# Optimization experiments

Hardware: AMD Instinct MI355X
Metric: run time of the kernel (lower is better)

Reference implementation:

```python
import jax, jax.numpy as jnp
import numpy as np

N_RAYS = 4096
WORLD_LEN = 160
K0_DIM = 12
WIDTH = 128
VIEWPE = 4
BG_LEN = 0.2
XYZ_MIN = -1.0 - BG_LEN
XYZ_MAX = 1.0 + BG_LEN
ALPHA_INIT = 1e-4
ACT_SHIFT = float(np.log(1.0 / (1.0 - ALPHA_INIT) - 1.0))  # density bias shift
BG = 1.0  # background color (render_kwargs['bg'])
DIM0 = 3 + 3 * VIEWPE * 2 + K0_DIM  # 39


def grid_interp(grid, pts):
    """Trilinear interpolation (align_corners=True). grid: [C,R,R,R], pts: [M,3] world coords -> [M,C]."""
    R = grid.shape[1]
    g = (pts - XYZ_MIN) / (XYZ_MAX - XYZ_MIN) * (R - 1)
    g = jnp.clip(g, 0.0, R - 1)
    g0 = jnp.clip(jnp.floor(g).astype(jnp.int32), 0, R - 2)
    f = g - g0
    x0, y0, z0 = g0[:, 0], g0[:, 1], g0[:, 2]
    fx, fy, fz = f[:, 0], f[:, 1], f[:, 2]

    def gat(i, j, k):
        return grid[:, i, j, k]  # [C, M]

    c00 = gat(x0, y0, z0) * (1 - fz) + gat(x0, y0, z0 + 1) * fz
    c01 = gat(x0, y0 + 1, z0) * (1 - fz) + gat(x0, y0 + 1, z0 + 1) * fz
    c10 = gat(x0 + 1, y0, z0) * (1 - fz) + gat(x0 + 1, y0, z0 + 1) * fz
    c11 = gat(x0 + 1, y0 + 1, z0) * (1 - fz) + gat(x0 + 1, y0 + 1, z0 + 1) * fz
    c0 = c00 * (1 - fy) + c01 * fy
    c1 = c10 * (1 - fy) + c11 * fy
    return (c0 * (1 - fx) + c1 * fx).T  # [M, C]


def setup_inputs() -> dict:
    key = jax.random.key(0)
    ks = jax.random.split(key, 11)
    return {
        "rays_o": jax.random.normal(ks[0], (N_RAYS, 3), jnp.float32) * 0.3,
        "rays_d": jax.random.normal(ks[1], (N_RAYS, 3), jnp.float32),
        "viewdirs": jax.random.normal(ks[2], (N_RAYS, 3), jnp.float32),
        "density_grid": jax.random.normal(ks[3], (1, WORLD_LEN, WORLD_LEN, WORLD_LEN), jnp.float32),
        "k0_grid": jax.random.normal(ks[4], (K0_DIM, WORLD_LEN, WORLD_LEN, WORLD_LEN), jnp.float32),
        "w0": jax.random.normal(ks[5], (DIM0, WIDTH), jnp.float32) * 0.05,
        "b0": jnp.zeros((WIDTH,), jnp.float32),
        "w1": jax.random.normal(ks[6], (WIDTH, WIDTH), jnp.float32) * 0.05,
        "b1": jnp.zeros((WIDTH,), jnp.float32),
        "w2": jax.random.normal(ks[7], (WIDTH, 3), jnp.float32) * 0.05,
        "b2": jnp.zeros((3,), jnp.float32),
        "stepsize": 1,
    }


def reference(rays_o, rays_d, viewdirs, density_grid, k0_grid, w0, b0, w1, b1, w2, b2, stepsize):
    sqrt3 = float(np.sqrt(3.0))
    # --- sample_ray: sample points along rays in the contracted domain ---
    N_inner = int(2.0 / (2.0 + 2.0 * BG_LEN) * sqrt3 * WORLD_LEN / stepsize) + 1
    N_outer = int(N_inner * max(0.01, BG_LEN / 2.0))
    b_inner = jnp.linspace(0.0, 2.0 * sqrt3, N_inner + 1)
    b_outer = 2.0 * sqrt3 / jnp.linspace(1.0, 0.001, N_outer + 1)
    t = jnp.concatenate([(b_inner[1:] + b_inner[:-1]) * 0.5,
                         (b_outer[1:] + b_outer[:-1]) * 0.5])  # [P]
    # scene_center = 0, scene_radius = 1 for xyz_min=-1, xyz_max=1
    rd = rays_d / jnp.linalg.norm(rays_d, axis=-1, keepdims=True)
    pts = rays_o[:, None, :] + rd[:, None, :] * t[None, :, None]  # [N,P,3]
    norm = jnp.max(jnp.abs(pts), axis=-1, keepdims=True)
    safe = jnp.maximum(norm, 1e-9)
    pts = jnp.where(norm <= 1.0, pts, pts / safe * (1.0 + BG_LEN - BG_LEN / safe))
    N, P = pts.shape[0], pts.shape[1]
    flat = pts.reshape(-1, 3)  # [M,3]

    # --- density -> alpha (Raw2Alpha); mask_cache is all-True, fast_color_thres=0 ---
    interval = float(stepsize) * 1.0  # voxel_size_ratio == 1
    dens = grid_interp(density_grid, flat)[:, 0].reshape(N, P)
    alpha = 1.0 - jnp.power(1.0 + jnp.exp(dens + ACT_SHIFT), -interval)

    # --- Alphas2Weights: per-ray alpha compositing ---
    T = jnp.cumprod(1.0 - alpha, axis=1)
    T_excl = jnp.concatenate([jnp.ones((N, 1), T.dtype), T[:, :-1]], axis=1)
    weights = alpha * T_excl  # [N,P]
    alphainv_last = T[:, -1]  # [N]

    # --- k0 features + view-dependent MLP ---
    k0 = grid_interp(k0_grid, flat).reshape(N, P, K0_DIM)
    vf = (2.0 ** jnp.arange(VIEWPE)).astype(rays_o.dtype)
    ve = (viewdirs[..., None] * vf).reshape(N, -1)
    vemb = jnp.concatenate([viewdirs, jnp.sin(ve), jnp.cos(ve)], axis=-1)  # [N, 3+24]
    feat = jnp.concatenate(
        [k0, jnp.broadcast_to(vemb[:, None, :], (N, P, vemb.shape[-1]))], axis=-1)  # [N,P,39]
    h = jax.nn.relu(feat @ w0 + b0)
    h = jax.nn.relu(h @ w1 + b1)
    rgb = jax.nn.sigmoid(h @ w2 + b2)  # [N,P,3]

    # --- volume rendering ---
    rgb_marched = jnp.sum(weights[..., None] * rgb, axis=1) + alphainv_last[:, None] * BG
    return rgb_marched  # [N,3]
```

## Files before the change

### kernel.cpp

```cpp
#include <hip/hip_runtime.h>

#define NRAYS 4096
#define PSAMP 254
#define NIN   231
#define GR    160
#define GR2   25600
#define GR3   4096000
#define SROW  136

typedef __attribute__((ext_vector_type(8))) short bf16x8;
typedef __attribute__((ext_vector_type(4))) float f32x4;

__device__ __forceinline__ unsigned short f2bf(float x) {
    union { float f; unsigned u; } v; v.f = x;
    return (unsigned short)((v.u + 0x7fffu + ((v.u >> 16) & 1u)) >> 16);
}
__device__ __forceinline__ float sigmoidf_(float x) { return 1.0f / (1.0f + __expf(-x)); }

__device__ __forceinline__ unsigned cvt_pk_bf16(float a, float b) {
    unsigned r;
    asm("v_cvt_pk_bf16_f32 %0, %1, %2" : "=v"(r) : "v"(a), "v"(b));
    return r;
}

__device__ __forceinline__ unsigned packh2(float a, float b) {
    union { _Float16 h; unsigned short u; } ua, ub;
    ua.h = (_Float16)a; ub.h = (_Float16)b;
    return (unsigned)ua.u | ((unsigned)ub.u << 16);
}
__device__ __forceinline__ float h2f(unsigned u16) {
    union { unsigned short u; _Float16 h; } v; v.u = (unsigned short)u16;
    return (float)v.h;
}
__device__ __forceinline__ float cget(const uint4& q, int c) {
    const unsigned w = ((const unsigned*)&q)[c >> 1];
    return h2f((c & 1) ? (w >> 16) : (w & 0xffffu));
}

__global__ void prepack(const float* __restrict__ w, unsigned short* __restrict__ out,
                        int K, int N, int ldw, int NT, int KS) {
    const int idx = blockIdx.x * 256 + threadIdx.x;
    if (idx >= NT * KS * 64) return;
    const int l  = idx & 63, f = idx >> 6;
    const int ks = f % KS,  nt = f / KS;
    const int n  = nt * 16 + (l & 15);
    const int k0 = ks * 32 + (l >> 4) * 8;
    unsigned p[4];
    #pragma unroll
    for (int q = 0; q < 4; q++) {
        const int ka = k0 + 2 * q, kb = ka + 1;
        const float va = (ka < K && n < N) ? w[ka * ldw + n] : 0.0f;
        const float vb = (kb < K && n < N) ? w[kb * ldw + n] : 0.0f;
        p[q] = (unsigned)f2bf(va) | ((unsigned)f2bf(vb) << 16);
    }
    uint4 v; v.x = p[0]; v.y = p[1]; v.z = p[2]; v.w = p[3];
    ((uint4*)out)[idx] = v;
}

__global__ __launch_bounds__(256) void repack_grid(
    const float* __restrict__ dg, const float* __restrict__ k0g,
    unsigned short* __restrict__ pg)
{
    const int i2 = blockIdx.x * 256 + threadIdx.x;
    if (i2 >= GR3 / 2) return;
    unsigned ow[16];
    #pragma unroll
    for (int c = 0; c < 12; c += 2) {
        const float2 va = ((const float2*)(k0g + (size_t)c       * GR3))[i2];
        const float2 vb = ((const float2*)(k0g + (size_t)(c + 1) * GR3))[i2];
        ow[(c >> 1)]     = packh2(va.x, vb.x);
        ow[8 + (c >> 1)] = packh2(va.y, vb.y);
    }
    const float2 dv = ((const float2*)dg)[i2];
    ow[6]  = packh2(dv.x, 0.0f);
    ow[14] = packh2(dv.y, 0.0f);
    ow[7] = 0u; ow[15] = 0u;
    uint4* dst = (uint4*)(pg + (size_t)i2 * 32);
    dst[0] = make_uint4(ow[0],  ow[1],  ow[2],  ow[3]);
    dst[1] = make_uint4(ow[4],  ow[5],  ow[6],  ow[7]);
    dst[2] = make_uint4(ow[8],  ow[9],  ow[10], ow[11]);
    dst[3] = make_uint4(ow[12], ow[13], ow[14], ow[15]);
}

__global__ __launch_bounds__(256, 2) void voxgo_mfma_pk(
    const float* __restrict__ rays_o, const float* __restrict__ rays_d,
    const float* __restrict__ viewdirs,
    const unsigned short* __restrict__ pg,
    const float* __restrict__ b0, const float* __restrict__ b1,
    const float* __restrict__ b2,
    const unsigned short* __restrict__ pw0, const unsigned short* __restrict__ pw1,
    const unsigned short* __restrict__ pw2,
    float* __restrict__ out)
{
    const int r    = blockIdx.x;
    const int tid  = threadIdx.x;
    const int wv   = tid >> 6, lane = tid & 63, quad = lane >> 4, l16 = lane & 15;

    __shared__ unsigned short hbuf[4][64 * SROW];
    __shared__ float wgt[256];
    __shared__ float redbuf[4 * 16 * 3];
    __shared__ float wtot[4];

    const float ox = rays_o[3*r+0], oy = rays_o[3*r+1], oz = rays_o[3*r+2];
    float dxv = rays_d[3*r+0], dyv = rays_d[3*r+1], dzv = rays_d[3*r+2];
    const float vdx = viewdirs[3*r+0], vdy = viewdirs[3*r+1], vdz = viewdirs[3*r+2];
    const float rinv = rsqrtf(dxv*dxv + dyv*dyv + dzv*dzv);
    dxv *= rinv; dyv *= rinv; dzv *= rinv;

    float t;
    if (tid < NIN) {
        t = ((float)tid + 0.5f) * (2.0f * 1.7320508075688772f / 231.0f);
    } else {
        const float lstep = 0.999f / 23.0f;
        const int j = tid - NIN;
        const float L0 = 1.0f - (float)j * lstep;
        const float L1 = 1.0f - (float)(j+1) * lstep;
        t = 1.7320508075688772f * (1.0f/L0 + 1.0f/L1);
    }

    float px = fmaf(dxv, t, ox), py = fmaf(dyv, t, oy), pz = fmaf(dzv, t, oz);
    const float nrm = fmaxf(fabsf(px), fmaxf(fabsf(py), fabsf(pz)));
    if (nrm > 1.0f) {
        const float s = (1.2f - 0.2f / nrm) / nrm;
        px *= s; py *= s; pz *= s;
    }

    const float gsc = 159.0f / 2.4f;
    const float gx = fminf(fmaxf((px + 1.2f) * gsc, 0.0f), 159.0f);
    const float gy = fminf(fmaxf((py + 1.2f) * gsc, 0.0f), 159.0f);
    const float gz = fminf(fmaxf((pz + 1.2f) * gsc, 0.0f), 159.0f);
    const int x0 = min((int)gx, GR-2), y0 = min((int)gy, GR-2), z0 = min((int)gz, GR-2);
    const float fx = gx - (float)x0, fy = gy - (float)y0, fz = gz - (float)z0;
    const int base = x0*GR2 + y0*GR + z0;

    const unsigned short* cp = pg + (size_t)base * 16;
    uint4 hi[8], lo[8];
    #pragma unroll
    for (int j = 0; j < 8; j++) {
        const int off = ((j >> 2) * GR2 + ((j >> 1) & 1) * GR + (j & 1)) * 16;
        hi[j] = *((const uint4*)(cp + off) + 1);
    }
    #pragma unroll
    for (int j = 0; j < 8; j++) {
        const int off = ((j >> 2) * GR2 + ((j >> 1) & 1) * GR + (j & 1)) * 16;
        lo[j] = *((const uint4*)(cp + off));
    }

    float fv[40];
    fv[12] = vdx; fv[13] = vdy; fv[14] = vdz;
    #pragma unroll
    for (int p = 0; p < 4; p++) {
        const float f = (float)(1 << p);
        fv[15+p] = __sinf(vdx*f);  fv[19+p] = __sinf(vdy*f);  fv[23+p] = __sinf(vdz*f);
        fv[27+p] = __cosf(vdx*f);  fv[31+p] = __cosf(vdy*f);  fv[35+p] = __cosf(vdz*f);
    }
    fv[39] = 0.0f;

    float dcr[8];
    #pragma unroll
    for (int j = 0; j < 8; j++) dcr[j] = h2f(hi[j].z & 0xffffu);
    const float c00 = dcr[0]*(1.0f-fz) + dcr[1]*fz;
    const float c01 = dcr[2]*(1.0f-fz) + dcr[3]*fz;
    const float c10 = dcr[4]*(1.0f-fz) + dcr[5]*fz;
    const float c11 = dcr[6]*(1.0f-fz) + dcr[7]*fz;
    const float dens = (c00*(1.0f-fy) + c01*fy)*(1.0f-fx) + (c10*(1.0f-fy) + c11*fy)*fx;

    const float ACT_SHIFT = -9.21024036697535f;
    const float alpha = (tid < PSAMP) ? sigmoidf_(dens + ACT_SHIFT) : 0.0f;

    float vscan = 1.0f - alpha;
    #pragma unroll
    for (int off = 1; off < 64; off <<= 1) {
        const float u = __shfl_up(vscan, off);
        if (lane >= off) vscan *= u;
    }
    if (lane == 63) wtot[wv] = vscan;
    __syncthreads();
    float pre = 1.0f;
    #pragma unroll
    for (int w = 0; w < 3; w++) if (w < wv) pre *= wtot[w];
    const float eprev = __shfl_up(vscan, 1);
    const float T_excl = (lane == 0) ? pre : pre * eprev;
    wgt[tid] = alpha * T_excl;

    const float wx0 = 1.0f-fx, wy0 = 1.0f-fy, wz0 = 1.0f-fz;
    const float w000 = wx0*wy0*wz0, w001 = wx0*wy0*fz, w010 = wx0*fy*wz0, w011 = wx0*fy*fz;
    const float w100 = fx*wy0*wz0,  w101 = fx*wy0*fz,  w110 = fx*fy*wz0,  w111 = fx*fy*fz;

    #pragma unroll
    for (int c = 0; c < 12; c++) {
        float s;
        if (c < 8) {
            s = w000*cget(lo[0],c) + w001*cget(lo[1],c)
              + w010*cget(lo[2],c) + w011*cget(lo[3],c)
              + w100*cget(lo[4],c) + w101*cget(lo[5],c)
              + w110*cget(lo[6],c) + w111*cget(lo[7],c);
        } else {
            s = w000*cget(hi[0],c-8) + w001*cget(hi[1],c-8)
              + w010*cget(hi[2],c-8) + w011*cget(hi[3],c-8)
              + w100*cget(hi[4],c-8) + w101*cget(hi[5],c-8)
              + w110*cget(hi[6],c-8) + w111*cget(hi[7],c-8);
        }
        fv[c] = s;
    }

    unsigned short* hb = &hbuf[wv][0];
    {
        const int row = tid & 63;
        uint4* dst = (uint4*)(hb + row * SROW);
        #pragma unroll
        for (int i = 0; i < 8; i++) {
            unsigned p[4];
            #pragma unroll
            for (int q = 0; q < 4; q++) {
                const int e0 = i*8 + 2*q, e1 = e0 + 1;
                const float a = (e0 < 39) ? fv[e0] : 0.0f;
                const float b = (e1 < 39) ? fv[e1] : 0.0f;
                p[q] = cvt_pk_bf16(a, b);
            }
            uint4 v; v.x = p[0]; v.y = p[1]; v.z = p[2]; v.w = p[3];
            dst[i] = v;
        }
    }


    f32x4 acc1[8][4];
    #pragma unroll
    for (int ft = 0; ft < 8; ft++) {
        const f32x4 bv = *(const f32x4*)(b0 + ft*16 + quad*4);
        #pragma unroll
        for (int st = 0; st < 4; st++) acc1[ft][st] = bv;
    }
    #pragma unroll
    for (int ks = 0; ks < 2; ks++) {
        bf16x8 bfr[4];
        #pragma unroll
        for (int st = 0; st < 4; st++)
            bfr[st] = *(const bf16x8*)(hb + (st*16 + l16)*SROW + ks*32 + quad*8);
        #pragma unroll
        for (int ft = 0; ft < 8; ft++) {
            const bf16x8 afr = *(const bf16x8*)(pw0 + ((ft*2 + ks)*64 + lane)*8);
            #pragma unroll
            for (int st = 0; st < 4; st++)
                acc1[ft][st] = __builtin_amdgcn_mfma_f32_16x16x32_bf16(afr, bfr[st], acc1[ft][st], 0,0,0);
        }
    }
    #pragma unroll
    for (int ft = 0; ft < 8; ft++)
        #pragma unroll
        for (int st = 0; st < 4; st++) {
            const f32x4 a = acc1[ft][st];
            uint2 v;
            v.x = cvt_pk_bf16(fmaxf(a[0], 0.0f), fmaxf(a[1], 0.0f));
            v.y = cvt_pk_bf16(fmaxf(a[2], 0.0f), fmaxf(a[3], 0.0f));
            *(uint2*)(hb + (st*16 + l16)*SROW + ft*16 + quad*4) = v;
        }

    f32x4 acc2[8][4];
    #pragma unroll
    for (int ft = 0; ft < 8; ft++) {
        const f32x4 bv = *(const f32x4*)(b1 + ft*16 + quad*4);
        #pragma unroll
        for (int st = 0; st < 4; st++) acc2[ft][st] = bv;
    }
    #pragma unroll
    for (int ks = 0; ks < 4; ks++) {
        bf16x8 bfr[4];
        #pragma unroll
        for (int st = 0; st < 4; st++)
            bfr[st] = *(const bf16x8*)(hb + (st*16 + l16)*SROW + ks*32 + quad*8);
        #pragma unroll
        for (int ft = 0; ft < 8; ft++) {
            const bf16x8 afr = *(const bf16x8*)(pw1 + ((ft*4 + ks)*64 + lane)*8);
            #pragma unroll
            for (int st = 0; st < 4; st++)
                acc2[ft][st] = __builtin_amdgcn_mfma_f32_16x16x32_bf16(afr, bfr[st], acc2[ft][st], 0,0,0);
        }
    }
    #pragma unroll
    for (int ft = 0; ft < 8; ft++)
        #pragma unroll
        for (int st = 0; st < 4; st++) {
            const f32x4 a = acc2[ft][st];
            uint2 v;
            v.x = cvt_pk_bf16(fmaxf(a[0], 0.0f), fmaxf(a[1], 0.0f));
            v.y = cvt_pk_bf16(fmaxf(a[2], 0.0f), fmaxf(a[3], 0.0f));
            *(uint2*)(hb + (st*16 + l16)*SROW + ft*16 + quad*4) = v;
        }

    f32x4 acc3[4];
    {
        f32x4 bz3; bz3[0] = b2[0]; bz3[1] = b2[1]; bz3[2] = b2[2]; bz3[3] = 0.0f;
        #pragma unroll
        for (int st = 0; st < 4; st++) acc3[st] = bz3;
    }
    #pragma unroll
    for (int ks = 0; ks < 4; ks++) {
        const bf16x8 afr = *(const bf16x8*)(pw2 + (ks*64 + lane)*8);
        #pragma unroll
        for (int st = 0; st < 4; st++) {
            const bf16x8 bfr = *(const bf16x8*)(hb + (st*16 + l16)*SROW + ks*32 + quad*8);
            acc3[st] = __builtin_amdgcn_mfma_f32_16x16x32_bf16(afr, bfr, acc3[st], 0,0,0);
        }
    }

    if (quad == 0) {
        float c0 = 0.0f, c1 = 0.0f, c2 = 0.0f;
        #pragma unroll
        for (int st = 0; st < 4; st++) {
            const float w = wgt[wv*64 + st*16 + l16];
            c0 += w * sigmoidf_(acc3[st][0]);
            c1 += w * sigmoidf_(acc3[st][1]);
            c2 += w * sigmoidf_(acc3[st][2]);
        }
        float* rb = &redbuf[(wv*16 + l16)*3];
        rb[0] = c0; rb[1] = c1; rb[2] = c2;
    }
    __syncthreads();
    if (tid < 3) {
        float acc_o = wtot[0]*wtot[1]*wtot[2]*wtot[3];
        #pragma unroll 4
        for (int i = 0; i < 64; i++) acc_o += redbuf[i*3 + tid];
        out[3*r + tid] = acc_o;
    }
}

__global__ __launch_bounds__(256, 2) void voxgo_mfma_f32(
    const float* __restrict__ rays_o, const float* __restrict__ rays_d,
    const float* __restrict__ viewdirs, const float* __restrict__ dg,
    const float* __restrict__ k0g,
    const float* __restrict__ b0, const float* __restrict__ b1,
    const float* __restrict__ b2,
    const unsigned short* __restrict__ pw0, const unsigned short* __restrict__ pw1,
    const unsigned short* __restrict__ pw2,
    float* __restrict__ out)
{
    const int r    = blockIdx.x;
    const int tid  = threadIdx.x;
    const int wv   = tid >> 6, lane = tid & 63, quad = lane >> 4, l16 = lane & 15;

    __shared__ unsigned short hbuf[4][64 * SROW];
    __shared__ float sc[256];
    __shared__ float wgt[256];
    __shared__ float redbuf[256];

    const float ox = rays_o[3*r+0], oy = rays_o[3*r+1], oz = rays_o[3*r+2];
    float dxv = rays_d[3*r+0], dyv = rays_d[3*r+1], dzv = rays_d[3*r+2];
    const float vdx = viewdirs[3*r+0], vdy = viewdirs[3*r+1], vdz = viewdirs[3*r+2];
    const float rinv = rsqrtf(dxv*dxv + dyv*dyv + dzv*dzv);
    dxv *= rinv; dyv *= rinv; dzv *= rinv;

    float t;
    if (tid < NIN) {
        t = ((float)tid + 0.5f) * (2.0f * 1.7320508075688772f / 231.0f);
    } else {
        const float lstep = 0.999f / 23.0f;
        const int j = tid - NIN;
        const float L0 = 1.0f - (float)j * lstep;
        const float L1 = 1.0f - (float)(j+1) * lstep;
        t = 1.7320508075688772f * (1.0f/L0 + 1.0f/L1);
    }

    float px = fmaf(dxv, t, ox), py = fmaf(dyv, t, oy), pz = fmaf(dzv, t, oz);
    const float nrm = fmaxf(fabsf(px), fmaxf(fabsf(py), fabsf(pz)));
    if (nrm > 1.0f) {
        const float s = (1.2f - 0.2f / nrm) / nrm;
        px *= s; py *= s; pz *= s;
    }

    const float gsc = 159.0f / 2.4f;
    const float gx = fminf(fmaxf((px + 1.2f) * gsc, 0.0f), 159.0f);
    const float gy = fminf(fmaxf((py + 1.2f) * gsc, 0.0f), 159.0f);
    const float gz = fminf(fmaxf((pz + 1.2f) * gsc, 0.0f), 159.0f);
    const int x0 = min((int)gx, GR-2), y0 = min((int)gy, GR-2), z0 = min((int)gz, GR-2);
    const float fx = gx - (float)x0, fy = gy - (float)y0, fz = gz - (float)z0;
    const int base = x0*GR2 + y0*GR + z0;

    const float d000 = dg[base],        d001 = dg[base+1];
    const float d010 = dg[base+GR],     d011 = dg[base+GR+1];
    const float d100 = dg[base+GR2],    d101 = dg[base+GR2+1];
    const float d110 = dg[base+GR2+GR], d111 = dg[base+GR2+GR+1];
    const float c00 = d000*(1.0f-fz) + d001*fz;
    const float c01 = d010*(1.0f-fz) + d011*fz;
    const float c10 = d100*(1.0f-fz) + d101*fz;
    const float c11 = d110*(1.0f-fz) + d111*fz;
    const float dens = (c00*(1.0f-fy) + c01*fy)*(1.0f-fx) + (c10*(1.0f-fy) + c11*fy)*fx;

    const float ACT_SHIFT = -9.21024036697535f;
    const float alpha = (tid < PSAMP) ? sigmoidf_(dens + ACT_SHIFT) : 0.0f;

    sc[tid] = 1.0f - alpha;
    __syncthreads();
    #pragma unroll
    for (int off = 1; off < 256; off <<= 1) {
        const float v = (tid >= off) ? sc[tid - off] : 1.0f;
        __syncthreads();
        sc[tid] *= v;
        __syncthreads();
    }
    const float T_excl = (tid == 0) ? 1.0f : sc[tid-1];
    wgt[tid] = alpha * T_excl;

    const float wx0 = 1.0f-fx, wy0 = 1.0f-fy, wz0 = 1.0f-fz;
    const float w000 = wx0*wy0*wz0, w001 = wx0*wy0*fz, w010 = wx0*fy*wz0, w011 = wx0*fy*fz;
    const float w100 = fx*wy0*wz0,  w101 = fx*wy0*fz,  w110 = fx*fy*wz0,  w111 = fx*fy*fz;

    float fv[40];
    #pragma unroll
    for (int c = 0; c < 12; c++) {
        const float* g = k0g + c*GR3 + base;
        fv[c] = w000*g[0]      + w001*g[1]
              + w010*g[GR]     + w011*g[GR+1]
              + w100*g[GR2]    + w101*g[GR2+1]
              + w110*g[GR2+GR] + w111*g[GR2+GR+1];
    }
    fv[12] = vdx; fv[13] = vdy; fv[14] = vdz;
    #pragma unroll
    for (int p = 0; p < 4; p++) {
        const float f = (float)(1 << p);
        fv[15+p] = __sinf(vdx*f);  fv[19+p] = __sinf(vdy*f);  fv[23+p] = __sinf(vdz*f);
        fv[27+p] = __cosf(vdx*f);  fv[31+p] = __cosf(vdy*f);  fv[35+p] = __cosf(vdz*f);
    }
    fv[39] = 0.0f;

    unsigned short* hb = &hbuf[wv][0];
    {
        const int row = tid & 63;
        uint4* dst = (uint4*)(hb + row * SROW);
        #pragma unroll
        for (int i = 0; i < 8; i++) {
            unsigned p[4];
            #pragma unroll
            for (int q = 0; q < 4; q++) {
                const int e0 = i*8 + 2*q, e1 = e0 + 1;
                const unsigned lov = (e0 < 39) ? f2bf(fv[e0]) : 0u;
                const unsigned hiv = (e1 < 39) ? f2bf(fv[e1]) : 0u;
                p[q] = lov | (hiv << 16);
            }
            uint4 v; v.x = p[0]; v.y = p[1]; v.z = p[2]; v.w = p[3];
            dst[i] = v;
        }
    }
    __syncthreads();

    f32x4 acc1[4][8];
    #pragma unroll
    for (int nt = 0; nt < 8; nt++) {
        const float bz = b0[nt*16 + l16];
        #pragma unroll
        for (int mt = 0; mt < 4; mt++) { f32x4 z = {bz,bz,bz,bz}; acc1[mt][nt] = z; }
    }
    #pragma unroll
    for (int ks = 0; ks < 2; ks++) {
        bf16x8 a[4];
        #pragma unroll
        for (int mt = 0; mt < 4; mt++)
            a[mt] = *(const bf16x8*)(hb + (mt*16 + l16)*SROW + ks*32 + quad*8);
        #pragma unroll
        for (int nt = 0; nt < 8; nt++) {
            const bf16x8 b = *(const bf16x8*)(pw0 + ((nt*2 + ks)*64 + lane)*8);
            #pragma unroll
            for (int mt = 0; mt < 4; mt++)
                acc1[mt][nt] = __builtin_amdgcn_mfma_f32_16x16x32_bf16(a[mt], b, acc1[mt][nt], 0,0,0);
        }
    }
    #pragma unroll
    for (int mt = 0; mt < 4; mt++)
        #pragma unroll
        for (int nt = 0; nt < 8; nt++)
            #pragma unroll
            for (int e = 0; e < 4; e++)
                hb[(mt*16 + quad*4 + e)*SROW + nt*16 + l16] = f2bf(fmaxf(acc1[mt][nt][e], 0.0f));
    __syncthreads();

    f32x4 acc2[4][8];
    #pragma unroll
    for (int nt = 0; nt < 8; nt++) {
        const float bz = b1[nt*16 + l16];
        #pragma unroll
        for (int mt = 0; mt < 4; mt++) { f32x4 z = {bz,bz,bz,bz}; acc2[mt][nt] = z; }
    }
    #pragma unroll
    for (int ks = 0; ks < 4; ks++) {
        bf16x8 a[4];
        #pragma unroll
        for (int mt = 0; mt < 4; mt++)
            a[mt] = *(const bf16x8*)(hb + (mt*16 + l16)*SROW + ks*32 + quad*8);
        #pragma unroll
        for (int nt = 0; nt < 8; nt++) {
            const bf16x8 b = *(const bf16x8*)(pw1 + ((nt*4 + ks)*64 + lane)*8);
            #pragma unroll
            for (int mt = 0; mt < 4; mt++)
                acc2[mt][nt] = __builtin_amdgcn_mfma_f32_16x16x32_bf16(a[mt], b, acc2[mt][nt], 0,0,0);
        }
    }
    #pragma unroll
    for (int mt = 0; mt < 4; mt++)
        #pragma unroll
        for (int nt = 0; nt < 8; nt++)
            #pragma unroll
            for (int e = 0; e < 4; e++)
                hb[(mt*16 + quad*4 + e)*SROW + nt*16 + l16] = f2bf(fmaxf(acc2[mt][nt][e], 0.0f));
    __syncthreads();

    f32x4 acc3[4];
    {
        const float bz = (l16 < 3) ? b2[l16] : 0.0f;
        #pragma unroll
        for (int mt = 0; mt < 4; mt++) { f32x4 z = {bz,bz,bz,bz}; acc3[mt] = z; }
    }
    #pragma unroll
    for (int ks = 0; ks < 4; ks++) {
        const bf16x8 b = *(const bf16x8*)(pw2 + (ks*64 + lane)*8);
        #pragma unroll
        for (int mt = 0; mt < 4; mt++) {
            const bf16x8 a = *(const bf16x8*)(hb + (mt*16 + l16)*SROW + ks*32 + quad*8);
            acc3[mt] = __builtin_amdgcn_mfma_f32_16x16x32_bf16(a, b, acc3[mt], 0,0,0);
        }
    }

    float contrib = 0.0f;
    #pragma unroll
    for (int mt = 0; mt < 4; mt++)
        #pragma unroll
        for (int e = 0; e < 4; e++) {
            const float s = sigmoidf_(acc3[mt][e]);
            contrib += wgt[wv*64 + mt*16 + quad*4 + e] * s;
        }
    redbuf[tid] = contrib;
    __syncthreads();
    if (tid < 3) {
        float acc_o = sc[PSAMP-1];
        #pragma unroll
        for (int w = 0; w < 4; w++)
            #pragma unroll
            for (int q = 0; q < 4; q++)
                acc_o += redbuf[w*64 + q*16 + tid];
        out[3*r + tid] = acc_o;
    }
}

extern "C" void kernel_launch(void* const* d_in, const int* in_sizes, int n_in,
                              void* d_out, int out_size, void* d_ws, size_t ws_size,
                              hipStream_t stream) {
    (void)in_sizes; (void)n_in; (void)out_size;
    const size_t PG_BYTES = (size_t)GR3 * 32;
    const size_t PW_BYTES = (size_t)(16 + 32 + 4) * 64 * 8 * 2;

    if (ws_size >= PG_BYTES + PW_BYTES) {
        unsigned short* pg  = (unsigned short*)d_ws;
        unsigned short* pw0 = (unsigned short*)((char*)d_ws + PG_BYTES);
        unsigned short* pw1 = pw0 + 16*64*8;
        unsigned short* pw2 = pw1 + 32*64*8;

        repack_grid<<<GR3/512, 256, 0, stream>>>(
            (const float*)d_in[3], (const float*)d_in[4], pg);
        prepack<<<4, 256, 0, stream>>>((const float*)d_in[5], pw0,  39, 128, 128, 8, 2);
        prepack<<<8, 256, 0, stream>>>((const float*)d_in[7], pw1, 128, 128, 128, 8, 4);
        prepack<<<1, 256, 0, stream>>>((const float*)d_in[9], pw2, 128,   3,   3, 1, 4);

        voxgo_mfma_pk<<<NRAYS, 256, 0, stream>>>(
            (const float*)d_in[0], (const float*)d_in[1], (const float*)d_in[2],
            pg,
            (const float*)d_in[6], (const float*)d_in[8], (const float*)d_in[10],
            pw0, pw1, pw2,
            (float*)d_out);
    } else {
        unsigned short* pw0 = (unsigned short*)d_ws;
        unsigned short* pw1 = pw0 + 16*64*8;
        unsigned short* pw2 = pw1 + 32*64*8;

        prepack<<<4, 256, 0, stream>>>((const float*)d_in[5], pw0,  39, 128, 128, 8, 2);
        prepack<<<8, 256, 0, stream>>>((const float*)d_in[7], pw1, 128, 128, 128, 8, 4);
        prepack<<<1, 256, 0, stream>>>((const float*)d_in[9], pw2, 128,   3,   3, 1, 4);

        voxgo_mfma_f32<<<NRAYS, 256, 0, stream>>>(
            (const float*)d_in[0], (const float*)d_in[1], (const float*)d_in[2],
            (const float*)d_in[3], (const float*)d_in[4],
            (const float*)d_in[6], (const float*)d_in[8], (const float*)d_in[10],
            pw0, pw1, pw2,
            (float*)d_out);
    }
}
```

Baseline: 438.4 us.

## Switch MLP to fp16 MFMA with packed-half interpolation and XOR-swizzled LDS

Converts the packed-grid kernel path from bf16 to fp16. Weights are prepacked as half, the MLP uses the 16x16x32 f16 MFMA, and activations are packed with v_cvt_pkrtz. The k0 trilinear interpolation now runs as packed half2 multiply-adds directly on the fp16 grid words instead of per-channel float conversions. The padded LDS row stride is replaced by a 256-byte row with an XOR swizzle to avoid bank conflicts. The aim is fewer ALU conversion instructions and less LDS footprint, at the cost of fp16 accumulation error in the interpolation and round-toward-zero on activations.

Result: no change. 440.7 us, median of 2 (+0.5%).

```diff
diff --git a/kernel.cpp b/kernel.cpp
--- a/kernel.cpp
+++ b/kernel.cpp
@@ -9,6 +9,8 @@
 #define SROW  136
 
 typedef __attribute__((ext_vector_type(8))) short bf16x8;
+typedef __attribute__((ext_vector_type(8))) _Float16 f16x8;
+typedef __attribute__((ext_vector_type(2))) _Float16 h2;
 typedef __attribute__((ext_vector_type(4))) float f32x4;
 
 __device__ __forceinline__ unsigned short f2bf(float x) {
@@ -16,12 +18,6 @@
     return (unsigned short)((v.u + 0x7fffu + ((v.u >> 16) & 1u)) >> 16);
 }
 __device__ __forceinline__ float sigmoidf_(float x) { return 1.0f / (1.0f + __expf(-x)); }
-
-__device__ __forceinline__ unsigned cvt_pk_bf16(float a, float b) {
-    unsigned r;
-    asm("v_cvt_pk_bf16_f32 %0, %1, %2" : "=v"(r) : "v"(a), "v"(b));
-    return r;
-}
 
 __device__ __forceinline__ unsigned packh2(float a, float b) {
     union { _Float16 h; unsigned short u; } ua, ub;
@@ -32,13 +28,17 @@
     union { unsigned short u; _Float16 h; } v; v.u = (unsigned short)u16;
     return (float)v.h;
 }
-__device__ __forceinline__ float cget(const uint4& q, int c) {
-    const unsigned w = ((const unsigned*)&q)[c >> 1];
-    return h2f((c & 1) ? (w >> 16) : (w & 0xffffu));
+__device__ __forceinline__ unsigned pkrtz(float a, float b) {
+    unsigned r;
+    asm("v_cvt_pkrtz_f16_f32 %0, %1, %2" : "=v"(r) : "v"(a), "v"(b));
+    return r;
+}
+__device__ __forceinline__ h2 u2h(unsigned u) {
+    union { unsigned u; h2 h; } v; v.u = u; return v.h;
 }
 
 __global__ void prepack(const float* __restrict__ w, unsigned short* __restrict__ out,
-                        int K, int N, int ldw, int NT, int KS) {
+                        int K, int N, int ldw, int NT, int KS, int f16mode) {
     const int idx = blockIdx.x * 256 + threadIdx.x;
     if (idx >= NT * KS * 64) return;
     const int l  = idx & 63, f = idx >> 6;
@@ -51,7 +51,8 @@
         const int ka = k0 + 2 * q, kb = ka + 1;
         const float va = (ka < K && n < N) ? w[ka * ldw + n] : 0.0f;
         const float vb = (kb < K && n < N) ? w[kb * ldw + n] : 0.0f;
-        p[q] = (unsigned)f2bf(va) | ((unsigned)f2bf(vb) << 16);
+        p[q] = f16mode ? packh2(va, vb)
+                       : ((unsigned)f2bf(va) | ((unsigned)f2bf(vb) << 16));
     }
     uint4 v; v.x = p[0]; v.y = p[1]; v.z = p[2]; v.w = p[3];
     ((uint4*)out)[idx] = v;
@@ -96,7 +97,7 @@
     const int tid  = threadIdx.x;
     const int wv   = tid >> 6, lane = tid & 63, quad = lane >> 4, l16 = lane & 15;
 
-    __shared__ unsigned short hbuf[4][64 * SROW];
+    __shared__ unsigned short hbuf[4][64 * 128];
     __shared__ float wgt[256];
     __shared__ float redbuf[4 * 16 * 3];
     __shared__ float wtot[4];
@@ -146,15 +147,15 @@
         lo[j] = *((const uint4*)(cp + off));
     }
 
-    float fv[40];
-    fv[12] = vdx; fv[13] = vdy; fv[14] = vdz;
+    float vv[28];
+    vv[0] = vdx; vv[1] = vdy; vv[2] = vdz;
     #pragma unroll
     for (int p = 0; p < 4; p++) {
         const float f = (float)(1 << p);
-        fv[15+p] = __sinf(vdx*f);  fv[19+p] = __sinf(vdy*f);  fv[23+p] = __sinf(vdz*f);
-        fv[27+p] = __cosf(vdx*f);  fv[31+p] = __cosf(vdy*f);  fv[35+p] = __cosf(vdz*f);
-    }
-    fv[39] = 0.0f;
+        vv[3+p]  = __sinf(vdx*f);  vv[7+p]  = __sinf(vdy*f);  vv[11+p] = __sinf(vdz*f);
+        vv[15+p] = __cosf(vdx*f);  vv[19+p] = __cosf(vdy*f);  vv[23+p] = __cosf(vdz*f);
+    }
+    vv[27] = 0.0f;
 
     float dcr[8];
     #pragma unroll
@@ -184,45 +185,45 @@
     wgt[tid] = alpha * T_excl;
 
     const float wx0 = 1.0f-fx, wy0 = 1.0f-fy, wz0 = 1.0f-fz;
-    const float w000 = wx0*wy0*wz0, w001 = wx0*wy0*fz, w010 = wx0*fy*wz0, w011 = wx0*fy*fz;
-    const float w100 = fx*wy0*wz0,  w101 = fx*wy0*fz,  w110 = fx*fy*wz0,  w111 = fx*fy*fz;
-
-    #pragma unroll
-    for (int c = 0; c < 12; c++) {
-        float s;
-        if (c < 8) {
-            s = w000*cget(lo[0],c) + w001*cget(lo[1],c)
-              + w010*cget(lo[2],c) + w011*cget(lo[3],c)
-              + w100*cget(lo[4],c) + w101*cget(lo[5],c)
-              + w110*cget(lo[6],c) + w111*cget(lo[7],c);
-        } else {
-            s = w000*cget(hi[0],c-8) + w001*cget(hi[1],c-8)
-              + w010*cget(hi[2],c-8) + w011*cget(hi[3],c-8)
-              + w100*cget(hi[4],c-8) + w101*cget(hi[5],c-8)
-              + w110*cget(hi[6],c-8) + w111*cget(hi[7],c-8);
-        }
-        fv[c] = s;
-    }
+    h2 wpk[8];
+    #pragma unroll
+    for (int j = 0; j < 8; j++) {
+        const float wj = ((j & 4) ? fx : wx0) * ((j & 2) ? fy : wy0) * ((j & 1) ? fz : wz0);
+        const _Float16 wh = (_Float16)wj;
+        h2 w2v; w2v[0] = wh; w2v[1] = wh; wpk[j] = w2v;
+    }
+    h2 ap[6];
+    #pragma unroll
+    for (int p = 0; p < 6; p++) { h2 z; z[0] = (_Float16)0.0f; z[1] = (_Float16)0.0f; ap[p] = z; }
+    #pragma unroll
+    for (int j = 0; j < 8; j++) {
+        ap[0] += wpk[j] * u2h(lo[j].x);
+        ap[1] += wpk[j] * u2h(lo[j].y);
+        ap[2] += wpk[j] * u2h(lo[j].z);
+        ap[3] += wpk[j] * u2h(lo[j].w);
+        ap[4] += wpk[j] * u2h(hi[j].x);
+        ap[5] += wpk[j] * u2h(hi[j].y);
+    }
+
+    unsigned fw[32];
+    #pragma unroll
+    for (int p = 0; p < 6; p++) { union { h2 h; unsigned u; } v; v.h = ap[p]; fw[p] = v.u; }
+    #pragma unroll
+    for (int i = 0; i < 14; i++) fw[6+i] = pkrtz(vv[2*i], vv[2*i+1]);
+    #pragma unroll
+    for (int i = 20; i < 32; i++) fw[i] = 0u;
 
     unsigned short* hb = &hbuf[wv][0];
+    const unsigned swr = (unsigned)((l16 & 7) << 4);
     {
         const int row = tid & 63;
-        uint4* dst = (uint4*)(hb + row * SROW);
+        const unsigned sw = (unsigned)((row & 7) << 4);
         #pragma unroll
         for (int i = 0; i < 8; i++) {
-            unsigned p[4];
-            #pragma unroll
-            for (int q = 0; q < 4; q++) {
-                const int e0 = i*8 + 2*q, e1 = e0 + 1;
-                const float a = (e0 < 39) ? fv[e0] : 0.0f;
-                const float b = (e1 < 39) ? fv[e1] : 0.0f;
-                p[q] = cvt_pk_bf16(a, b);
-            }
-            uint4 v; v.x = p[0]; v.y = p[1]; v.z = p[2]; v.w = p[3];
-            dst[i] = v;
-        }
-    }
-
+            uint4 v; v.x = fw[4*i]; v.y = fw[4*i+1]; v.z = fw[4*i+2]; v.w = fw[4*i+3];
+            *(uint4*)((char*)hb + row*256 + ((unsigned)(i*16) ^ sw)) = v;
+        }
+    }
 
     f32x4 acc1[8][4];
     #pragma unroll
@@ -233,16 +234,17 @@
     }
     #pragma unroll
     for (int ks = 0; ks < 2; ks++) {
-        bf16x8 bfr[4];
+        f16x8 bfr[4];
         #pragma unroll
         for (int st = 0; st < 4; st++)
-            bfr[st] = *(const bf16x8*)(hb + (st*16 + l16)*SROW + ks*32 + quad*8);
+            bfr[st] = *(const f16x8*)((char*)hb + (st*16 + l16)*256
+                                      + ((unsigned)(ks*64 + quad*16) ^ swr));
         #pragma unroll
         for (int ft = 0; ft < 8; ft++) {
-            const bf16x8 afr = *(const bf16x8*)(pw0 + ((ft*2 + ks)*64 + lane)*8);
+            const f16x8 afr = *(const f16x8*)(pw0 + ((ft*2 + ks)*64 + lane)*8);
             #pragma unroll
             for (int st = 0; st < 4; st++)
-                acc1[ft][st] = __builtin_amdgcn_mfma_f32_16x16x32_bf16(afr, bfr[st], acc1[ft][st], 0,0,0);
+                acc1[ft][st] = __builtin_amdgcn_mfma_f32_16x16x32_f16(afr, bfr[st], acc1[ft][st], 0,0,0);
         }
     }
     #pragma unroll
@@ -251,9 +253,9 @@
         for (int st = 0; st < 4; st++) {
             const f32x4 a = acc1[ft][st];
             uint2 v;
-            v.x = cvt_pk_bf16(fmaxf(a[0], 0.0f), fmaxf(a[1], 0.0f));
-            v.y = cvt_pk_bf16(fmaxf(a[2], 0.0f), fmaxf(a[3], 0.0f));
-            *(uint2*)(hb + (st*16 + l16)*SROW + ft*16 + quad*4) = v;
+            v.x = pkrtz(fmaxf(a[0], 0.0f), fmaxf(a[1], 0.0f));
+            v.y = pkrtz(fmaxf(a[2], 0.0f), fmaxf(a[3], 0.0f));
+            *(uint2*)((char*)hb + (st*16 + l16)*256 + ((unsigned)(ft*32 + quad*8) ^ swr)) = v;
         }
 
     f32x4 acc2[8][4];
@@ -265,16 +267,17 @@
     }
     #pragma unroll
     for (int ks = 0; ks < 4; ks++) {
-        bf16x8 bfr[4];
+        f16x8 bfr[4];
         #pragma unroll
         for (int st = 0; st < 4; st++)
-            bfr[st] = *(const bf16x8*)(hb + (st*16 + l16)*SROW + ks*32 + quad*8);
+            bfr[st] = *(const f16x8*)((char*)hb + (st*16 + l16)*256
+                                      + ((unsigned)(ks*64 + quad*16) ^ swr));
         #pragma unroll
         for (int ft = 0; ft < 8; ft++) {
-            const bf16x8 afr = *(const bf16x8*)(pw1 + ((ft*4 + ks)*64 + lane)*8);
+            const f16x8 afr = *(const f16x8*)(pw1 + ((ft*4 + ks)*64 + lane)*8);
             #pragma unroll
             for (int st = 0; st < 4; st++)
-                acc2[ft][st] = __builtin_amdgcn_mfma_f32_16x16x32_bf16(afr, bfr[st], acc2[ft][st], 0,0,0);
+                acc2[ft][st] = __builtin_amdgcn_mfma_f32_16x16x32_f16(afr, bfr[st], acc2[ft][st], 0,0,0);
         }
     }
     #pragma unroll
@@ -283,9 +286,9 @@
         for (int st = 0; st < 4; st++) {
             const f32x4 a = acc2[ft][st];
             uint2 v;
-            v.x = cvt_pk_bf16(fmaxf(a[0], 0.0f), fmaxf(a[1], 0.0f));
-            v.y = cvt_pk_bf16(fmaxf(a[2], 0.0f), fmaxf(a[3], 0.0f));
-            *(uint2*)(hb + (st*16 + l16)*SROW + ft*16 + quad*4) = v;
+            v.x = pkrtz(fmaxf(a[0], 0.0f), fmaxf(a[1], 0.0f));
+            v.y = pkrtz(fmaxf(a[2], 0.0f), fmaxf(a[3], 0.0f));
+            *(uint2*)((char*)hb + (st*16 + l16)*256 + ((unsigned)(ft*32 + quad*8) ^ swr)) = v;
         }
 
     f32x4 acc3[4];
@@ -296,11 +299,12 @@
     }
     #pragma unroll
     for (int ks = 0; ks < 4; ks++) {
-        const bf16x8 afr = *(const bf16x8*)(pw2 + (ks*64 + lane)*8);
+        const f16x8 afr = *(const f16x8*)(pw2 + (ks*64 + lane)*8);
         #pragma unroll
         for (int st = 0; st < 4; st++) {
-            const bf16x8 bfr = *(const bf16x8*)(hb + (st*16 + l16)*SROW + ks*32 + quad*8);
-            acc3[st] = __builtin_amdgcn_mfma_f32_16x16x32_bf16(afr, bfr, acc3[st], 0,0,0);
+            const f16x8 bfr = *(const f16x8*)((char*)hb + (st*16 + l16)*256
+                                              + ((unsigned)(ks*64 + quad*16) ^ swr));
+            acc3[st] = __builtin_amdgcn_mfma_f32_16x16x32_f16(afr, bfr, acc3[st], 0,0,0);
         }
     }
 
@@ -555,9 +559,9 @@
 
         repack_grid<<<GR3/512, 256, 0, stream>>>(
             (const float*)d_in[3], (const float*)d_in[4], pg);
-        prepack<<<4, 256, 0, stream>>>((const float*)d_in[5], pw0,  39, 128, 128, 8, 2);
-        prepack<<<8, 256, 0, stream>>>((const float*)d_in[7], pw1, 128, 128, 128, 8, 4);
-        prepack<<<1, 256, 0, stream>>>((const float*)d_in[9], pw2, 128,   3,   3, 1, 4);
+        prepack<<<4, 256, 0, stream>>>((const float*)d_in[5], pw0,  39, 128, 128, 8, 2, 1);
+        prepack<<<8, 256, 0, stream>>>((const float*)d_in[7], pw1, 128, 128, 128, 8, 4, 1);
+        prepack<<<1, 256, 0, stream>>>((const float*)d_in[9], pw2, 128,   3,   3, 1, 4, 1);
 
         voxgo_mfma_pk<<<NRAYS, 256, 0, stream>>>(
             (const float*)d_in[0], (const float*)d_in[1], (const float*)d_in[2],
@@ -570,9 +574,9 @@
         unsigned short* pw1 = pw0 + 16*64*8;
         unsigned short* pw2 = pw1 + 32*64*8;
 
-        prepack<<<4, 256, 0, stream>>>((const float*)d_in[5], pw0,  39, 128, 128, 8, 2);
-        prepack<<<8, 256, 0, stream>>>((const float*)d_in[7], pw1, 128, 128, 128, 8, 4);
-        prepack<<<1, 256, 0, stream>>>((const float*)d_in[9], pw2, 128,   3,   3, 1, 4);
+        prepack<<<4, 256, 0, stream>>>((const float*)d_in[5], pw0,  39, 128, 128, 8, 2, 0);
+        prepack<<<8, 256, 0, stream>>>((const float*)d_in[7], pw1, 128, 128, 128, 8, 4, 0);
+        prepack<<<1, 256, 0, stream>>>((const float*)d_in[9], pw2, 128,   3,   3, 1, 4, 0);
 
         voxgo_mfma_f32<<<NRAYS, 256, 0, stream>>>(
             (const float*)d_in[0], (const float*)d_in[1], (const float*)d_in[2],
```
